# Performance work log

Hardware: AMD Instinct MI355X
Metric: run time of the kernel (lower is better)

The kernel has to match this reference:

```python
import jax, jax.numpy as jnp
import numpy as np

N = 100000
NEG_SLOPE = 0.2
EPS = 1e-16


def gat_conv(x, edge_index, W, att_src, att_dst, bias, concat):
    # x: [N, Fin]; W: [Fin, H*C]; att_*: [H, C]; edge_index: [2, E] (with self loops)
    H, C = att_src.shape
    src, dst = edge_index[0], edge_index[1]
    h = (x @ W).reshape(-1, H, C)                       # [N, H, C]
    a_src = (h * att_src).sum(-1)                       # [N, H]
    a_dst = (h * att_dst).sum(-1)                       # [N, H]
    e = a_src[src] + a_dst[dst]                         # [E, H]
    e = jnp.where(e >= 0, e, NEG_SLOPE * e)             # LeakyReLU(0.2)
    # segment softmax over destination-node neighborhoods
    m = jax.ops.segment_max(e, dst, num_segments=N)     # [N, H]
    ex = jnp.exp(e - m[dst])
    denom = jax.ops.segment_sum(ex, dst, num_segments=N)
    alpha = ex / (denom[dst] + EPS)                     # [E, H]
    msg = h[src] * alpha[:, :, None]                    # [E, H, C]
    out = jax.ops.segment_sum(msg, dst, num_segments=N)  # [N, H, C]
    out = out.reshape(N, H * C) if concat else out.mean(axis=1)
    return out + bias


def setup_inputs() -> dict:
    key = jax.random.key(0)
    ks = jax.random.split(key, 10)
    Fin, Ch, Co, Hh = 256, 32, 64, 4
    E = 1600000
    x = jax.random.normal(ks[0], (N, Fin), dtype=jnp.float32)
    edge_index = jax.random.randint(ks[1], (2, E), 0, N, dtype=jnp.int64)
    s1 = 1.0 / np.sqrt(Fin)
    s2 = 1.0 / np.sqrt(Hh * Ch)
    W1 = jax.random.normal(ks[2], (Fin, Hh * Ch), dtype=jnp.float32) * s1
    att_src1 = jax.random.normal(ks[3], (Hh, Ch), dtype=jnp.float32) * (1.0 / np.sqrt(Ch))
    att_dst1 = jax.random.normal(ks[4], (Hh, Ch), dtype=jnp.float32) * (1.0 / np.sqrt(Ch))
    b1 = jnp.zeros((Hh * Ch,), dtype=jnp.float32)
    W2 = jax.random.normal(ks[5], (Hh * Ch, Co), dtype=jnp.float32) * s2
    att_src2 = jax.random.normal(ks[6], (1, Co), dtype=jnp.float32) * (1.0 / np.sqrt(Co))
    att_dst2 = jax.random.normal(ks[7], (1, Co), dtype=jnp.float32) * (1.0 / np.sqrt(Co))
    b2 = jnp.zeros((Co,), dtype=jnp.float32)
    return {"x": x, "edge_index": edge_index,
            "W1": W1, "att_src1": att_src1, "att_dst1": att_dst1, "b1": b1,
            "W2": W2, "att_src2": att_src2, "att_dst2": att_dst2, "b2": b2}


def reference(x, edge_index, W1, att_src1, att_dst1, b1, W2, att_src2, att_dst2, b2):
    # add self-loops (PyG GATConv default add_self_loops=True)
    loops = jnp.arange(N, dtype=edge_index.dtype)
    ei = jnp.concatenate([edge_index, jnp.stack([loops, loops])], axis=1)
    h = gat_conv(x, ei, W1, att_src1, att_dst1, b1, concat=True)
    h = jax.nn.elu(h)
    out = gat_conv(h, ei, W2, att_src2, att_dst2, b2, concat=False)
    return out
```

## Files before the change

### kernel.cpp

```cpp
#include <hip/hip_runtime.h>
#include <math.h>

typedef unsigned short ushort_t;
typedef unsigned int uint_t;
typedef __attribute__((ext_vector_type(8))) short short8;
typedef __attribute__((ext_vector_type(4))) float fx4;
typedef __attribute__((ext_vector_type(16))) float f32x16;
typedef __attribute__((ext_vector_type(4))) uint_t uintx4;
typedef __attribute__((ext_vector_type(2))) uint_t uintx2;

__device__ __forceinline__ float bf16_to_f32(ushort_t u) {
    union { uint_t i; float f; } c;
    c.i = ((uint_t)u) << 16;
    return c.f;
}
__device__ __forceinline__ ushort_t f32_to_bf16(float f) {
    union { float f; uint_t i; } c;
    c.f = f;
    const uint_t x = c.i;
    return (ushort_t)((x + 0x7fffu + ((x >> 16) & 1u)) >> 16);
}
__device__ __forceinline__ void unpack_fma(uint_t w, float p, float& a0,
                                           float& a1) {
    union { uint_t i; float f; } lo, hi;
    lo.i = w << 16;
    hi.i = w & 0xffff0000u;
    a0 += p * lo.f;
    a1 += p * hi.f;
}

__global__ void convT2_kernel(const float* __restrict__ W1,
                              ushort_t* __restrict__ W1T,
                              const float* __restrict__ W2,
                              ushort_t* __restrict__ W2T) {
    const int idx = blockIdx.x * 256 + threadIdx.x;
    if (idx < 256 * 128) {
        const int mm = idx / 256;
        const int kk = idx - mm * 256;
        W1T[idx] = f32_to_bf16(W1[(size_t)kk * 128 + mm]);
    } else if (idx < 256 * 128 + 128 * 64) {
        const int j = idx - 256 * 128;
        const int mm = j / 128;
        const int kk = j - mm * 128;
        W2T[j] = f32_to_bf16(W2[(size_t)kk * 64 + mm]);
    }
}

template <int TILES32, bool A_F32, int K, int KS>
__global__ __launch_bounds__(256) void gemm32_kernel(
    const void* __restrict__ Avoid, const ushort_t* __restrict__ BT,
    ushort_t* __restrict__ C, int n) {
    constexpr int M = TILES32 * 32;
    constexpr int CHS = KS / 8;
    constexpr int NSTEP = KS / 16;
    constexpr int NTOT = K / 16;
    __shared__ ushort_t lds[M * KS];
    const int tid = threadIdx.x;
    const int wave = tid >> 6;
    const int lane = tid & 63;
    const int l31 = lane & 31;
    const int half = lane >> 5;
    const int rowbase = blockIdx.x * 256 + wave * 64;
    const int r0 = min(rowbase + l31, n - 1);
    const int r1 = min(rowbase + 32 + l31, n - 1);
    const size_t off0 = (size_t)r0 * K + half * 8;
    const size_t off1 = (size_t)r1 * K + half * 8;

    f32x16 acc[2][TILES32];
#pragma unroll
    for (int rp = 0; rp < 2; ++rp)
#pragma unroll
        for (int t = 0; t < TILES32; ++t)
#pragma unroll
            for (int i = 0; i < 16; ++i) acc[rp][t][i] = 0.f;

    fx4 c0a, c0b, c1a, c1b, n0a, n0b, n1a, n1b;
    short8 cb0, cb1, nb0, nb1;

    if constexpr (A_F32) {
        const float* A = (const float*)Avoid;
        c0a = *(const fx4*)(A + off0);
        c0b = *(const fx4*)(A + off0 + 4);
        c1a = *(const fx4*)(A + off1);
        c1b = *(const fx4*)(A + off1 + 4);
    } else {
        const ushort_t* A = (const ushort_t*)Avoid;
        cb0 = *(const short8*)(A + off0);
        cb1 = *(const short8*)(A + off1);
    }

#pragma unroll
    for (int ks = 0; ks < K; ks += KS) {
        if (ks) __syncthreads();
#pragma unroll
        for (int i = 0; i < (M * CHS + 255) / 256; ++i) {
            const int idx = tid + i * 256;
            if (idx < M * CHS) {
                const int row = idx / CHS;
                const int c = idx - row * CHS;
                *(short8*)&lds[(size_t)(row * CHS +
                                        (c ^ (row & (CHS - 1)))) * 8] =
                    *(const short8*)(BT + (size_t)row * K + ks + c * 8);
            }
        }
        __syncthreads();

#pragma unroll
        for (int kstep = 0; kstep < NSTEP; ++kstep) {
            const int kg = ks / 16 + kstep;
            if (kg + 1 < NTOT) {
                const int kd = (kg + 1) * 16;
                if constexpr (A_F32) {
                    const float* A = (const float*)Avoid;
                    n0a = *(const fx4*)(A + off0 + kd);
                    n0b = *(const fx4*)(A + off0 + kd + 4);
                    n1a = *(const fx4*)(A + off1 + kd);
                    n1b = *(const fx4*)(A + off1 + kd + 4);
                } else {
                    const ushort_t* A = (const ushort_t*)Avoid;
                    nb0 = *(const short8*)(A + off0 + kd);
                    nb1 = *(const short8*)(A + off1 + kd);
                }
            }
            short8 bf[TILES32];
#pragma unroll
            for (int t = 0; t < TILES32; ++t) {
                const int brow = t * 32 + l31;
                const int c = kstep * 2 + half;
                bf[t] = *(const short8*)&lds[(size_t)(brow * CHS +
                                                      (c ^ (brow &
                                                            (CHS - 1)))) * 8];
            }
            short8 af0, af1;
            if constexpr (A_F32) {
                union { short8 v; ushort_t u[8]; } u0, u1;
#pragma unroll
                for (int j = 0; j < 4; ++j) {
                    u0.u[j] = f32_to_bf16(c0a[j]);
                    u0.u[4 + j] = f32_to_bf16(c0b[j]);
                    u1.u[j] = f32_to_bf16(c1a[j]);
                    u1.u[4 + j] = f32_to_bf16(c1b[j]);
                }
                af0 = u0.v;
                af1 = u1.v;
            } else {
                af0 = cb0;
                af1 = cb1;
            }
#pragma unroll
            for (int t = 0; t < TILES32; ++t) {
                acc[0][t] = __builtin_amdgcn_mfma_f32_32x32x16_bf16(
                    af0, bf[t], acc[0][t], 0, 0, 0);
                acc[1][t] = __builtin_amdgcn_mfma_f32_32x32x16_bf16(
                    af1, bf[t], acc[1][t], 0, 0, 0);
            }
            if (kg + 1 < NTOT) {
                if constexpr (A_F32) {
                    c0a = n0a; c0b = n0b; c1a = n1a; c1b = n1b;
                } else {
                    cb0 = nb0; cb1 = nb1;
                }
            }
        }
    }

#pragma unroll
    for (int rp = 0; rp < 2; ++rp) {
        const int base_r = rowbase + rp * 32 + 4 * half;
#pragma unroll
        for (int t = 0; t < TILES32; ++t) {
            const int col = t * 32 + l31;
#pragma unroll
            for (int reg = 0; reg < 16; ++reg) {
                const int rr = base_r + (reg & 3) + 8 * (reg >> 2);
                if (rr < n)
                    C[(size_t)rr * M + col] = f32_to_bf16(acc[rp][t][reg]);
            }
        }
    }
}

template <int H, int C>
__global__ void att_kernel(const ushort_t* __restrict__ h,
                           const float* __restrict__ att_s,
                           const float* __restrict__ att_d,
                           float* __restrict__ as_, float* __restrict__ ad_,
                           int n) {
    const int idx = blockIdx.x * blockDim.x + threadIdx.x;
    if (idx >= n * H) return;
    const int node = idx / H;
    const int hh = idx % H;
    const ushort_t* hp = h + (size_t)node * H * C + hh * C;
    float s0 = 0.f, s1 = 0.f;
#pragma unroll
    for (int c = 0; c < C; ++c) {
        const float v = bf16_to_f32(hp[c]);
        s0 += v * att_s[hh * C + c];
        s1 += v * att_d[hh * C + c];
    }
    as_[idx] = s0;
    ad_[idx] = s1;
}

__global__ __launch_bounds__(1024) void hist_kernel(const int* __restrict__ dst,
                                                    int* __restrict__ histG,
                                                    int e, int chunk, int NB,
                                                    int G) {
    __shared__ int hl[512];
    for (int b = threadIdx.x; b < NB; b += 1024) hl[b] = 0;
    __syncthreads();
    const int g = blockIdx.x;
    const int lo = g * chunk;
    const int hi = min(lo + chunk, e);
    for (int i = lo + threadIdx.x; i < hi; i += 1024)
        atomicAdd(&hl[dst[i] >> 8], 1);
    __syncthreads();
    for (int b = threadIdx.x; b < NB; b += 1024) histG[b * G + g] = hl[b];
}

__global__ __launch_bounds__(1024) void scan1_kernel(const int* __restrict__ in,
                                                     int* __restrict__ out,
                                                     int* __restrict__ sums,
                                                     int n) {
    __shared__ int s[1024];
    const int t = threadIdx.x;
    const int i = blockIdx.x * 1024 + t;
    const int v = (i < n) ? in[i] : 0;
    s[t] = v;
    __syncthreads();
    for (int d = 1; d < 1024; d <<= 1) {
        const int x = (t >= d) ? s[t - d] : 0;
        __syncthreads();
        s[t] += x;
        __syncthreads();
    }
    if (i < n) out[i] = s[t] - v;
    if (t == 1023) sums[blockIdx.x] = s[1023];
}

__global__ __launch_bounds__(128) void scan2_kernel(int* sums, int nb) {
    __shared__ int s[128];
    const int t = threadIdx.x;
    const int v = (t < nb) ? sums[t] : 0;
    s[t] = v;
    __syncthreads();
    for (int d = 1; d < 128; d <<= 1) {
        const int x = (t >= d) ? s[t - d] : 0;
        __syncthreads();
        s[t] += x;
        __syncthreads();
    }
    if (t < nb) sums[t] = s[t] - v;
}

__global__ __launch_bounds__(1024) void scan3_kernel(int* __restrict__ out,
                                                     const int* __restrict__ sums,
                                                     int n) {
    const int i = blockIdx.x * 1024 + threadIdx.x;
    if (i < n) out[i] += sums[blockIdx.x];
}

__global__ __launch_bounds__(1024) void bin_kernel(const int* __restrict__ src,
                                                   const int* __restrict__ dst,
                                                   const int* __restrict__ base,
                                                   uint_t* __restrict__ binned,
                                                   int e, int chunk, int NB,
                                                   int G) {
    __shared__ int cur[512];
    const int g = blockIdx.x;
    for (int b = threadIdx.x; b < NB; b += 1024) cur[b] = base[b * G + g];
    __syncthreads();
    const int lo = g * chunk;
    const int hi = min(lo + chunk, e);
    for (int i = lo + threadIdx.x; i < hi; i += 1024) {
        const int d = dst[i];
        const int p = atomicAdd(&cur[d >> 8], 1);
        binned[p] = (uint_t)src[i] | ((uint_t)(d & 255) << 17);
    }
}

#define BUILD_CAP 6144
__global__ __launch_bounds__(256) void build_kernel(
    const uint_t* __restrict__ binned, const int* __restrict__ base,
    int* __restrict__ csr, int* __restrict__ deg, int* __restrict__ offs,
    int e, int n, int NB, int G) {
    __shared__ uint_t ep[BUILD_CAP];
    __shared__ int degL[256];
    __shared__ int offL[256];
    __shared__ int curL[256];
    const int b = blockIdx.x;
    const int tid = threadIdx.x;
    const int start = base[b * G];
    const int end = (b == NB - 1) ? e : base[(b + 1) * G];
    const int cnt = end - start;
    const bool stage = (cnt <= BUILD_CAP);
    degL[tid] = 0;
    if (stage)
        for (int i = tid; i < cnt; i += 256) ep[i] = binned[start + i];
    __syncthreads();
    if (stage) {
        for (int i = tid; i < cnt; i += 256)
            atomicAdd(&degL[ep[i] >> 17], 1);
    } else {
        for (int i = tid; i < cnt; i += 256)
            atomicAdd(&degL[binned[start + i] >> 17], 1);
    }
    __syncthreads();
    const int v = degL[tid];
    offL[tid] = v;
    __syncthreads();
    for (int d = 1; d < 256; d <<= 1) {
        const int x = (tid >= d) ? offL[tid - d] : 0;
        __syncthreads();
        offL[tid] += x;
        __syncthreads();
    }
    const int excl = offL[tid] - v;
    curL[tid] = excl;
    const int node = (b << 8) + tid;
    if (node < n) {
        deg[node] = v;
        offs[node] = start + excl;
    }
    __syncthreads();
    if (stage) {
        for (int i = tid; i < cnt; i += 256) {
            const uint_t pr = ep[i];
            const int p = atomicAdd(&curL[pr >> 17], 1);
            csr[start + p] = (int)(pr & 0x1FFFFu);
        }
    } else {
        for (int i = tid; i < cnt; i += 256) {
            const uint_t pr = binned[start + i];
            const int p = atomicAdd(&curL[pr >> 17], 1);
            csr[start + p] = (int)(pr & 0x1FFFFu);
        }
    }
}

template <int H, int C, bool DO_ELU, bool OUT_BF16>
__global__ __launch_bounds__(64) void agg_kernel(
    const ushort_t* __restrict__ h, const float* __restrict__ a_src,
    const float* __restrict__ a_dst, const int* __restrict__ csr,
    const int* __restrict__ offs, const int* __restrict__ deg,
    const float* __restrict__ bias, void* __restrict__ outv, int n) {
    constexpr int HC = H * C;
    constexpr int R = HC / 16;
    constexpr int RW = R / 2;
    constexpr int U = 4;
    const int lane = threadIdx.x;
    const int s = lane & 15;
    const int g = lane >> 4;
    const int dst = blockIdx.x * 4 + g;
    const int dstc = min(dst, n - 1);
    const int start = offs[dstc];
    const int dg = deg[dstc];
    const int ch0 = s * R;
    const int myh = (H > 1) ? (ch0 / C) : 0;
    const float advm = a_dst[dstc * H + myh];

    int dmax = dg;
    dmax = max(dmax, __shfl_xor(dmax, 16));
    dmax = max(dmax, __shfl_xor(dmax, 32));
    dmax = __builtin_amdgcn_readfirstlane(dmax);

    float acc[R];
#pragma unroll
    for (int r = 0; r < R; ++r) acc[r] = 0.f;
    float L = 0.f;

    {
        float e = a_src[dstc * H + myh] + advm;
        e = fmaxf(e, 0.2f * e);
        const float p = __expf(e);
        L += p;
        const ushort_t* hp = h + (size_t)((uint_t)dstc * HC) + ch0;
        if constexpr (RW == 4) {
            const uintx4 v = *(const uintx4*)hp;
#pragma unroll
            for (int w = 0; w < 4; ++w)
                unpack_fma(v[w], p, acc[2 * w], acc[2 * w + 1]);
        } else {
            const uintx2 v = *(const uintx2*)hp;
#pragma unroll
            for (int w = 0; w < 2; ++w)
                unpack_fma(v[w], p, acc[2 * w], acc[2 * w + 1]);
        }
    }

    const int dm1c = (dg > 0) ? dg - 1 : 0;

    for (int j0 = 0; j0 < dmax; j0 += U) {
        int sv[U];
#pragma unroll
        for (int u = 0; u < U; ++u)
            sv[u] = csr[start + min(j0 + u, dm1c)];
        float es[U];
#pragma unroll
        for (int u = 0; u < U; ++u) es[u] = a_src[sv[u] * H + myh];
        uint_t hv[U][RW];
#pragma unroll
        for (int u = 0; u < U; ++u) {
            const ushort_t* hp = h + (size_t)((uint_t)sv[u] * HC) + ch0;
            if constexpr (RW == 4) {
                const uintx4 v = *(const uintx4*)hp;
#pragma unroll
                for (int w = 0; w < 4; ++w) hv[u][w] = v[w];
            } else {
                const uintx2 v = *(const uintx2*)hp;
#pragma unroll
                for (int w = 0; w < 2; ++w) hv[u][w] = v[w];
            }
        }
        float p[U];
#pragma unroll
        for (int u = 0; u < U; ++u) {
            float e = es[u] + advm;
            e = fmaxf(e, 0.2f * e);
            const float pe = __expf(e);
            p[u] = (j0 + u < dg) ? pe : 0.f;
        }
#pragma unroll
        for (int u = 0; u < U; ++u) {
            L += p[u];
#pragma unroll
            for (int w = 0; w < RW; ++w)
                unpack_fma(hv[u][w], p[u], acc[2 * w], acc[2 * w + 1]);
        }
    }

    if (dst >= n) return;
    const float linv = 1.f / (L + 1e-16f);
    float r[R];
#pragma unroll
    for (int d = 0; d < R; ++d) {
        r[d] = acc[d] * linv + bias[ch0 + d];
        if (DO_ELU) r[d] = (r[d] > 0.f) ? r[d] : (__expf(r[d]) - 1.f);
    }
    if constexpr (OUT_BF16) {
        uintx4 o;
#pragma unroll
        for (int w = 0; w < 4; ++w)
            o[w] = (uint_t)f32_to_bf16(r[2 * w]) |
                   ((uint_t)f32_to_bf16(r[2 * w + 1]) << 16);
        *(uintx4*)((ushort_t*)outv + (size_t)dst * HC + ch0) = o;
    } else {
        fx4 o;
#pragma unroll
        for (int d = 0; d < 4; ++d) o[d] = r[d];
        *(fx4*)((float*)outv + (size_t)dst * HC + ch0) = o;
    }
}

extern "C" void kernel_launch(void* const* d_in, const int* in_sizes, int n_in,
                              void* d_out, int out_size, void* d_ws,
                              size_t ws_size, hipStream_t stream) {
    const float* x = (const float*)d_in[0];
    const int* ei = (const int*)d_in[1];
    const float* W1 = (const float*)d_in[2];
    const float* att_s1 = (const float*)d_in[3];
    const float* att_d1 = (const float*)d_in[4];
    const float* b1 = (const float*)d_in[5];
    const float* W2 = (const float*)d_in[6];
    const float* att_s2 = (const float*)d_in[7];
    const float* att_d2 = (const float*)d_in[8];
    const float* b2 = (const float*)d_in[9];

    const int N = in_sizes[0] / 256;
    const int E = in_sizes[1] / 2;
    const int* srcp = ei;
    const int* dstp = ei + E;

    const int NB = (N + 255) >> 8;
    const int G = 128;
    const int NBG = NB * G;
    const int chunk = (E + G - 1) / G;
    const int nbs = (NBG + 1023) / 1024;

    float* as1 = (float*)d_ws;
    float* ad1 = as1 + (size_t)N * 4;
    float* as2 = ad1 + (size_t)N * 4;
    float* ad2 = as2 + N;
    int* histG = (int*)(ad2 + N);
    int* base = histG + NBG;
    int* sums = base + NBG;
    int* deg = sums + 128;
    int* offs = deg + N;
    int* csr = offs + N;
    uint_t* binned = (uint_t*)(csr + E);
    ushort_t* h1 = (ushort_t*)binned;
    ushort_t* h2 = h1 + (size_t)N * 128;
    ushort_t* h1p = h2 + (size_t)N * 64;
    ushort_t* W1T = h1p + (size_t)N * 128;
    ushort_t* W2T = W1T + 128 * 256;

    convT2_kernel<<<(256 * 128 + 128 * 64 + 255) / 256, 256, 0, stream>>>(
        W1, W1T, W2, W2T);

    hist_kernel<<<G, 1024, 0, stream>>>(dstp, histG, E, chunk, NB, G);
    scan1_kernel<<<nbs, 1024, 0, stream>>>(histG, base, sums, NBG);
    scan2_kernel<<<1, 128, 0, stream>>>(sums, nbs);
    scan3_kernel<<<nbs, 1024, 0, stream>>>(base, sums, NBG);
    bin_kernel<<<G, 1024, 0, stream>>>(srcp, dstp, base, binned, E, chunk, NB,
                                       G);
    build_kernel<<<NB, 256, 0, stream>>>(binned, base, csr, deg, offs, E, N,
                                         NB, G);

    const int gblk = (N + 255) / 256;
    const int ablk = (N + 3) / 4;

    gemm32_kernel<4, true, 256, 128><<<gblk, 256, 0, stream>>>(x, W1T, h1, N);
    att_kernel<4, 32><<<(N * 4 + 255) / 256, 256, 0, stream>>>(h1, att_s1,
                                                               att_d1, as1,
                                                               ad1, N);
    agg_kernel<4, 32, true, true><<<ablk, 64, 0, stream>>>(h1, as1, ad1, csr,
                                                           offs, deg, b1, h1p,
                                                           N);

    gemm32_kernel<2, false, 128, 128><<<gblk, 256, 0, stream>>>(h1p, W2T, h2,
                                                                N);
    att_kernel<1, 64><<<(N + 255) / 256, 256, 0, stream>>>(h2, att_s2, att_d2,
                                                           as2, ad2, N);
    agg_kernel<1, 64, false, false><<<ablk, 64, 0, stream>>>(h2, as2, ad2,
                                                             csr, offs, deg,
                                                             b2, d_out, N);
}
```

Baseline: 385.4 us.

## Fuse weight conversion into histogram kernel and split layer-1 aggregation into three launches

The weight transpose/bf16 conversion is folded into extra blocks of the histogram kernel, which removes one kernel launch. The layer-1 aggregation is split into three launches over node ranges, passing explicit lo/hi bounds. The split adds launches and looks aimed at changing scheduling or cache behaviour. It may add overhead without a clear benefit.

```diff
diff --git a/kernel.cpp b/kernel.cpp
--- a/kernel.cpp
+++ b/kernel.cpp
@@ -27,23 +27,6 @@
     hi.i = w & 0xffff0000u;
     a0 += p * lo.f;
     a1 += p * hi.f;
-}
-
-__global__ void convT2_kernel(const float* __restrict__ W1,
-                              ushort_t* __restrict__ W1T,
-                              const float* __restrict__ W2,
-                              ushort_t* __restrict__ W2T) {
-    const int idx = blockIdx.x * 256 + threadIdx.x;
-    if (idx < 256 * 128) {
-        const int mm = idx / 256;
-        const int kk = idx - mm * 256;
-        W1T[idx] = f32_to_bf16(W1[(size_t)kk * 128 + mm]);
-    } else if (idx < 256 * 128 + 128 * 64) {
-        const int j = idx - 256 * 128;
-        const int mm = j / 128;
-        const int kk = j - mm * 128;
-        W2T[j] = f32_to_bf16(W2[(size_t)kk * 64 + mm]);
-    }
 }
 
 template <int TILES32, bool A_F32, int K, int KS>
@@ -202,10 +185,24 @@
     ad_[idx] = s1;
 }
 
-__global__ __launch_bounds__(1024) void hist_kernel(const int* __restrict__ dst,
-                                                    int* __restrict__ histG,
-                                                    int e, int chunk, int NB,
-                                                    int G) {
+__global__ __launch_bounds__(1024) void hist_kernel(
+    const int* __restrict__ dst, int* __restrict__ histG, int e, int chunk,
+    int NB, int G, const float* __restrict__ W1, ushort_t* __restrict__ W1T,
+    const float* __restrict__ W2, ushort_t* __restrict__ W2T) {
+    if (blockIdx.x >= (uint_t)G) {
+        const int idx = (blockIdx.x - G) * 1024 + threadIdx.x;
+        if (idx < 256 * 128) {
+            const int mm = idx / 256;
+            const int kk = idx - mm * 256;
+            W1T[idx] = f32_to_bf16(W1[(size_t)kk * 128 + mm]);
+        } else if (idx < 256 * 128 + 128 * 64) {
+            const int j = idx - 256 * 128;
+            const int mm = j / 128;
+            const int kk = j - mm * 128;
+            W2T[j] = f32_to_bf16(W2[(size_t)kk * 64 + mm]);
+        }
+        return;
+    }
     __shared__ int hl[512];
     for (int b = threadIdx.x; b < NB; b += 1024) hl[b] = 0;
     __syncthreads();
@@ -343,7 +340,8 @@
     const ushort_t* __restrict__ h, const float* __restrict__ a_src,
     const float* __restrict__ a_dst, const int* __restrict__ csr,
     const int* __restrict__ offs, const int* __restrict__ deg,
-    const float* __restrict__ bias, void* __restrict__ outv, int n) {
+    const float* __restrict__ bias, void* __restrict__ outv, int n0, int n1,
+    int n) {
     constexpr int HC = H * C;
     constexpr int R = HC / 16;
     constexpr int RW = R / 2;
@@ -351,7 +349,7 @@
     const int lane = threadIdx.x;
     const int s = lane & 15;
     const int g = lane >> 4;
-    const int dst = blockIdx.x * 4 + g;
+    const int dst = n0 + blockIdx.x * 4 + g;
     const int dstc = min(dst, n - 1);
     const int start = offs[dstc];
     const int dg = deg[dstc];
@@ -429,7 +427,7 @@
         }
     }
 
-    if (dst >= n) return;
+    if (dst >= n1) return;
     const float linv = 1.f / (L + 1e-16f);
     float r[R];
 #pragma unroll
@@ -494,10 +492,9 @@
     ushort_t* W1T = h1p + (size_t)N * 128;
     ushort_t* W2T = W1T + 128 * 256;
 
-    convT2_kernel<<<(256 * 128 + 128 * 64 + 255) / 256, 256, 0, stream>>>(
-        W1, W1T, W2, W2T);
-
-    hist_kernel<<<G, 1024, 0, stream>>>(dstp, histG, E, chunk, NB, G);
+    const int cvblk = (256 * 128 + 128 * 64 + 1023) / 1024;
+    hist_kernel<<<G + cvblk, 1024, 0, stream>>>(dstp, histG, E, chunk, NB, G,
+                                                W1, W1T, W2, W2T);
     scan1_kernel<<<nbs, 1024, 0, stream>>>(histG, base, sums, NBG);
     scan2_kernel<<<1, 128, 0, stream>>>(sums, nbs);
     scan3_kernel<<<nbs, 1024, 0, stream>>>(base, sums, NBG);
@@ -507,21 +504,27 @@
                                          NB, G);
 
     const int gblk = (N + 255) / 256;
-    const int ablk = (N + 3) / 4;
 
     gemm32_kernel<4, true, 256, 128><<<gblk, 256, 0, stream>>>(x, W1T, h1, N);
     att_kernel<4, 32><<<(N * 4 + 255) / 256, 256, 0, stream>>>(h1, att_s1,
                                                                att_d1, as1,
                                                                ad1, N);
-    agg_kernel<4, 32, true, true><<<ablk, 64, 0, stream>>>(h1, as1, ad1, csr,
-                                                           offs, deg, b1, h1p,
-                                                           N);
+    {
+        const int part = (N + 2) / 3;
+        for (int p = 0; p < 3; ++p) {
+            const int lo = p * part;
+            const int hi = min(lo + part, N);
+            if (hi > lo)
+                agg_kernel<4, 32, true, true>
+                    <<<(hi - lo + 3) / 4, 64, 0, stream>>>(
+                        h1, as1, ad1, csr, offs, deg, b1, h1p, lo, hi, N);
+        }
+    }
 
     gemm32_kernel<2, false, 128, 128><<<gblk, 256, 0, stream>>>(h1p, W2T, h2,
                                                                 N);
     att_kernel<1, 64><<<(N + 255) / 256, 256, 0, stream>>>(h2, att_s2, att_d2,
                                                            as2, ad2, N);
-    agg_kernel<1, 64, false, false><<<ablk, 64, 0, stream>>>(h2, as2, ad2,
-                                                             csr, offs, deg,
-                                                             b2, d_out, N);
-}
+    agg_kernel<1, 64, false, false><<<(N + 3) / 4, 64, 0, stream>>>(
+        h2, as2, ad2, csr, offs, deg, b2, d_out, 0, N, N);
+}
```

After: 394.8 us. 2.4% more time.

## Fold weight conversion and scan2 into neighbors; halve GEMM rows per wave

Applied to the files above, without the earlier changes.

The weight transpose/bf16 conversion now runs as extra blocks of the histogram kernel, and the single-block scan2 is removed: each scan3 block sums the preceding block totals itself with a wavefront shuffle reduction. This drops two kernel launches and their serialization gaps. Separately, the GEMM now processes 32 rows per wave instead of 64, doubling the grid and halving accumulator registers, which raises occupancy but reduces B-fragment reuse from LDS. The in-block reduction assumes at most 64 scan blocks.

```diff
diff --git a/kernel.cpp b/kernel.cpp
--- a/kernel.cpp
+++ b/kernel.cpp
@@ -27,23 +27,6 @@
     hi.i = w & 0xffff0000u;
     a0 += p * lo.f;
     a1 += p * hi.f;
-}
-
-__global__ void convT2_kernel(const float* __restrict__ W1,
-                              ushort_t* __restrict__ W1T,
-                              const float* __restrict__ W2,
-                              ushort_t* __restrict__ W2T) {
-    const int idx = blockIdx.x * 256 + threadIdx.x;
-    if (idx < 256 * 128) {
-        const int mm = idx / 256;
-        const int kk = idx - mm * 256;
-        W1T[idx] = f32_to_bf16(W1[(size_t)kk * 128 + mm]);
-    } else if (idx < 256 * 128 + 128 * 64) {
-        const int j = idx - 256 * 128;
-        const int mm = j / 128;
-        const int kk = j - mm * 128;
-        W2T[j] = f32_to_bf16(W2[(size_t)kk * 64 + mm]);
-    }
 }
 
 template <int TILES32, bool A_F32, int K, int KS>
@@ -60,33 +43,26 @@
     const int lane = tid & 63;
     const int l31 = lane & 31;
     const int half = lane >> 5;
-    const int rowbase = blockIdx.x * 256 + wave * 64;
+    const int rowbase = blockIdx.x * 128 + wave * 32;
     const int r0 = min(rowbase + l31, n - 1);
-    const int r1 = min(rowbase + 32 + l31, n - 1);
     const size_t off0 = (size_t)r0 * K + half * 8;
-    const size_t off1 = (size_t)r1 * K + half * 8;
-
-    f32x16 acc[2][TILES32];
-#pragma unroll
-    for (int rp = 0; rp < 2; ++rp)
-#pragma unroll
-        for (int t = 0; t < TILES32; ++t)
-#pragma unroll
-            for (int i = 0; i < 16; ++i) acc[rp][t][i] = 0.f;
-
-    fx4 c0a, c0b, c1a, c1b, n0a, n0b, n1a, n1b;
-    short8 cb0, cb1, nb0, nb1;
+
+    f32x16 acc[TILES32];
+#pragma unroll
+    for (int t = 0; t < TILES32; ++t)
+#pragma unroll
+        for (int i = 0; i < 16; ++i) acc[t][i] = 0.f;
+
+    fx4 c0a, c0b, n0a, n0b;
+    short8 cb0, nb0;
 
     if constexpr (A_F32) {
         const float* A = (const float*)Avoid;
         c0a = *(const fx4*)(A + off0);
         c0b = *(const fx4*)(A + off0 + 4);
-        c1a = *(const fx4*)(A + off1);
-        c1b = *(const fx4*)(A + off1 + 4);
     } else {
         const ushort_t* A = (const ushort_t*)Avoid;
         cb0 = *(const short8*)(A + off0);
-        cb1 = *(const short8*)(A + off1);
     }
 
 #pragma unroll
@@ -114,12 +90,9 @@
                     const float* A = (const float*)Avoid;
                     n0a = *(const fx4*)(A + off0 + kd);
                     n0b = *(const fx4*)(A + off0 + kd + 4);
-                    n1a = *(const fx4*)(A + off1 + kd);
-                    n1b = *(const fx4*)(A + off1 + kd + 4);
                 } else {
                     const ushort_t* A = (const ushort_t*)Avoid;
                     nb0 = *(const short8*)(A + off0 + kd);
-                    nb1 = *(const short8*)(A + off1 + kd);
                 }
             }
             short8 bf[TILES32];
@@ -131,51 +104,41 @@
                                                       (c ^ (brow &
                                                             (CHS - 1)))) * 8];
             }
-            short8 af0, af1;
+            short8 af0;
             if constexpr (A_F32) {
-                union { short8 v; ushort_t u[8]; } u0, u1;
+                union { short8 v; ushort_t u[8]; } u0;
 #pragma unroll
                 for (int j = 0; j < 4; ++j) {
                     u0.u[j] = f32_to_bf16(c0a[j]);
                     u0.u[4 + j] = f32_to_bf16(c0b[j]);
-                    u1.u[j] = f32_to_bf16(c1a[j]);
-                    u1.u[4 + j] = f32_to_bf16(c1b[j]);
                 }
                 af0 = u0.v;
-                af1 = u1.v;
             } else {
                 af0 = cb0;
-                af1 = cb1;
             }
 #pragma unroll
             for (int t = 0; t < TILES32; ++t) {
-                acc[0][t] = __builtin_amdgcn_mfma_f32_32x32x16_bf16(
-                    af0, bf[t], acc[0][t], 0, 0, 0);
-                acc[1][t] = __builtin_amdgcn_mfma_f32_32x32x16_bf16(
-                    af1, bf[t], acc[1][t], 0, 0, 0);
+                acc[t] = __builtin_amdgcn_mfma_f32_32x32x16_bf16(
+                    af0, bf[t], acc[t], 0, 0, 0);
             }
             if (kg + 1 < NTOT) {
                 if constexpr (A_F32) {
-                    c0a = n0a; c0b = n0b; c1a = n1a; c1b = n1b;
+                    c0a = n0a; c0b = n0b;
                 } else {
-                    cb0 = nb0; cb1 = nb1;
+                    cb0 = nb0;
                 }
             }
         }
     }
 
-#pragma unroll
-    for (int rp = 0; rp < 2; ++rp) {
-        const int base_r = rowbase + rp * 32 + 4 * half;
-#pragma unroll
-        for (int t = 0; t < TILES32; ++t) {
-            const int col = t * 32 + l31;
-#pragma unroll
-            for (int reg = 0; reg < 16; ++reg) {
-                const int rr = base_r + (reg & 3) + 8 * (reg >> 2);
-                if (rr < n)
-                    C[(size_t)rr * M + col] = f32_to_bf16(acc[rp][t][reg]);
-            }
+    const int base_r = rowbase + 4 * half;
+#pragma unroll
+    for (int t = 0; t < TILES32; ++t) {
+        const int col = t * 32 + l31;
+#pragma unroll
+        for (int reg = 0; reg < 16; ++reg) {
+            const int rr = base_r + (reg & 3) + 8 * (reg >> 2);
+            if (rr < n) C[(size_t)rr * M + col] = f32_to_bf16(acc[t][reg]);
         }
     }
 }
@@ -202,10 +165,24 @@
     ad_[idx] = s1;
 }
 
-__global__ __launch_bounds__(1024) void hist_kernel(const int* __restrict__ dst,
-                                                    int* __restrict__ histG,
-                                                    int e, int chunk, int NB,
-                                                    int G) {
+__global__ __launch_bounds__(1024) void hist_kernel(
+    const int* __restrict__ dst, int* __restrict__ histG, int e, int chunk,
+    int NB, int G, const float* __restrict__ W1, ushort_t* __restrict__ W1T,
+    const float* __restrict__ W2, ushort_t* __restrict__ W2T) {
+    if (blockIdx.x >= (uint_t)G) {
+        const int idx = (blockIdx.x - G) * 1024 + threadIdx.x;
+        if (idx < 256 * 128) {
+            const int mm = idx / 256;
+            const int kk = idx - mm * 256;
+            W1T[idx] = f32_to_bf16(W1[(size_t)kk * 128 + mm]);
+        } else if (idx < 256 * 128 + 128 * 64) {
+            const int j = idx - 256 * 128;
+            const int mm = j / 128;
+            const int kk = j - mm * 128;
+            W2T[j] = f32_to_bf16(W2[(size_t)kk * 64 + mm]);
+        }
+        return;
+    }
     __shared__ int hl[512];
     for (int b = threadIdx.x; b < NB; b += 1024) hl[b] = 0;
     __syncthreads();
@@ -238,26 +215,19 @@
     if (t == 1023) sums[blockIdx.x] = s[1023];
 }
 
-__global__ __launch_bounds__(128) void scan2_kernel(int* sums, int nb) {
-    __shared__ int s[128];
-    const int t = threadIdx.x;
-    const int v = (t < nb) ? sums[t] : 0;
-    s[t] = v;
-    __syncthreads();
-    for (int d = 1; d < 128; d <<= 1) {
-        const int x = (t >= d) ? s[t - d] : 0;
-        __syncthreads();
-        s[t] += x;
-        __syncthreads();
-    }
-    if (t < nb) sums[t] = s[t] - v;
-}
-
-__global__ __launch_bounds__(1024) void scan3_kernel(int* __restrict__ out,
-                                                     const int* __restrict__ sums,
-                                                     int n) {
+__global__ __launch_bounds__(1024) void scan3_kernel(
+    int* __restrict__ out, const int* __restrict__ sums, int n, int nb) {
+    __shared__ int offsh;
+    if (threadIdx.x < 64) {
+        const int t = threadIdx.x;
+        int v = (t < nb && t < (int)blockIdx.x) ? sums[t] : 0;
+#pragma unroll
+        for (int d = 1; d < 64; d <<= 1) v += __shfl_xor(v, d);
+        if (t == 0) offsh = v;
+    }
+    __syncthreads();
     const int i = blockIdx.x * 1024 + threadIdx.x;
-    if (i < n) out[i] += sums[blockIdx.x];
+    if (i < n) out[i] += offsh;
 }
 
 __global__ __launch_bounds__(1024) void bin_kernel(const int* __restrict__ src,
@@ -494,19 +464,17 @@
     ushort_t* W1T = h1p + (size_t)N * 128;
     ushort_t* W2T = W1T + 128 * 256;
 
-    convT2_kernel<<<(256 * 128 + 128 * 64 + 255) / 256, 256, 0, stream>>>(
-        W1, W1T, W2, W2T);
-
-    hist_kernel<<<G, 1024, 0, stream>>>(dstp, histG, E, chunk, NB, G);
+    const int cvblk = (256 * 128 + 128 * 64 + 1023) / 1024;
+    hist_kernel<<<G + cvblk, 1024, 0, stream>>>(dstp, histG, E, chunk, NB, G,
+                                                W1, W1T, W2, W2T);
     scan1_kernel<<<nbs, 1024, 0, stream>>>(histG, base, sums, NBG);
-    scan2_kernel<<<1, 128, 0, stream>>>(sums, nbs);
-    scan3_kernel<<<nbs, 1024, 0, stream>>>(base, sums, NBG);
+    scan3_kernel<<<nbs, 1024, 0, stream>>>(base, sums, NBG, nbs);
     bin_kernel<<<G, 1024, 0, stream>>>(srcp, dstp, base, binned, E, chunk, NB,
                                        G);
     build_kernel<<<NB, 256, 0, stream>>>(binned, base, csr, deg, offs, E, N,
                                          NB, G);
 
-    const int gblk = (N + 255) / 256;
+    const int gblk = (N + 127) / 128;
     const int ablk = (N + 3) / 4;
 
     gemm32_kernel<4, true, 256, 128><<<gblk, 256, 0, stream>>>(x, W1T, h1, N);
```

Result: no change. 382.8 us (-0.7%).
